# Kernel optimization log

Hardware: AMD Instinct MI355X
Metric: run time of the kernel (lower is better)

Reference implementation:

```python
import jax, jax.numpy as jnp
import numpy as np

EPS = 1e-4  # ReEig eigenvalue clamp threshold (standard SPDNet value)


def _eig_apply(X, fn):
    # symmetric eig, apply fn to eigenvalues, reconstruct: V diag(fn(w)) V^T
    w, v = jnp.linalg.eigh(X)
    return jnp.einsum('...ij,...j,...kj->...ik', v, fn(w), v)


def _congr(P, G, mode):
    # CongrG: G^{+/-1/2} P G^{+/-1/2}, G is a single [n,n] SPD matrix
    w, v = jnp.linalg.eigh(G)
    s = jnp.sqrt(w) if mode == 'pos' else 1.0 / jnp.sqrt(w)
    Gs = (v * s) @ v.T  # [n,n]
    return Gs @ P @ Gs


def setup_inputs() -> dict:
    key = jax.random.key(0)
    ks = jax.random.split(key, 8)
    B, win, band, n, h, n_mid = 512, 3, 9, 22, 27, 32
    # SPD input covariance-like matrices
    M = jax.random.normal(ks[0], (B, win, band, n, n), dtype=jnp.float32)
    x = M @ jnp.swapaxes(M, -1, -2) / n + 0.5 * jnp.eye(n, dtype=jnp.float32)
    # Stiefel BiMap weights (orthonormal columns)
    W1, _ = jnp.linalg.qr(jax.random.normal(ks[1], (h, n_mid, n_mid), dtype=jnp.float32))
    Q2, _ = jnp.linalg.qr(jax.random.normal(ks[2], (h, n_mid, n_mid), dtype=jnp.float32))
    W2 = Q2[..., :n]
    running_mean = jnp.eye(n, dtype=jnp.float32)
    Aw = jax.random.normal(ks[3], (n, n), dtype=jnp.float32)
    bn_weight = Aw @ Aw.T / n + jnp.eye(n, dtype=jnp.float32)
    conv_w = jax.random.normal(ks[4], (48, 1, win, band * n * n), dtype=jnp.float32) * 0.01
    conv_b = jnp.zeros((48,), dtype=jnp.float32)
    fc_w = jax.random.normal(ks[5], (4, 48), dtype=jnp.float32) * 0.1
    fc_b = jnp.zeros((4,), dtype=jnp.float32)
    return {"x": x, "W1": W1, "W2": W2, "running_mean": running_mean,
            "bn_weight": bn_weight, "conv_w": conv_w, "conv_b": conv_b,
            "fc_w": fc_w, "fc_b": fc_b}


def reference(x, W1, W2, running_mean, bn_weight, conv_w, conv_b, fc_w, fc_b):
    B, win, band, n, _ = x.shape
    h = win * band
    no1 = W1.shape[-1]
    X = x.reshape(B, h, n, n)
    # SPDIncreaseDim(n -> no1): E X E^T + diag([0]*n + [1]*(no1-n))
    pad = no1 - n
    X = jnp.pad(X, ((0, 0), (0, 0), (0, pad), (0, pad)))
    X = X + jnp.diag(jnp.concatenate([jnp.zeros(n), jnp.ones(pad)])).astype(x.dtype)
    # BiMap 1 (per-channel W^T X W) + ReEig
    P = jnp.einsum('hni,bhnm,hmj->bhij', W1, X, W1)
    P = _eig_apply(P, lambda w: jnp.maximum(w, EPS))
    # BiMap 2
    P = jnp.einsum('hni,bhnm,hmj->bhij', W2, P, W2)
    # BatchNormSPD (eval mode): center by running_mean, scale by weight
    P = _congr(P, running_mean, 'neg')
    P = _congr(P, bn_weight, 'pos')
    # ReEig + LogEig
    P = _eig_apply(P, lambda w: jnp.maximum(w, EPS))
    P = _eig_apply(P, jnp.log)
    x_vec = P.reshape(B, win, band * n * n)
    feat = jnp.einsum('bhw,chw->bc', x_vec, conv_w[:, 0]) + conv_b  # [B, 48]
    return feat @ fc_w.T + fc_b                       # [B, classes]
```

## Files before the change

### kernel.cpp

```cpp
#include <hip/hip_runtime.h>


#define WS_CONST 484
#define WS_VT    512
#define WS_V     (512 + 13068)
#define WS_D     (13580 + 14256)
#define WS_G     (27836 + 13068)
#define G_STRIDE 528
#define V_STRIDE 528

typedef float v2f __attribute__((ext_vector_type(2)));

static __device__ __forceinline__ float dpp_shl1(float x) {
  return __int_as_float(__builtin_amdgcn_mov_dpp(__float_as_int(x), 0x101, 0xf, 0xf, true));
}
static __device__ __forceinline__ float dpp_shr1(float x) {
  return __int_as_float(__builtin_amdgcn_mov_dpp(__float_as_int(x), 0x111, 0xf, 0xf, true));
}

static __device__ __forceinline__ void jacobi_sweeps(v2f wl[11], v2f wr[11],
                                                     bool is0, bool is10, bool inert,
                                                     int minsweep, float eps2) {
  int okprev = 0;
  #pragma unroll 1
  for (int sweep = 0; sweep < 5; ++sweep) {
    if (sweep >= minsweep && __all(okprev)) break;
    v2f na = (v2f)(0.f), nb = (v2f)(0.f);
    #pragma unroll
    for (int i = 0; i < 11; ++i) { na += wl[i]*wl[i]; nb += wr[i]*wr[i]; }
    float nL = na.x + na.y, nR = nb.x + nb.y;
    float q = inert ? 0.f : (nL*nL + nR*nR);
    q += __shfl_xor(q, 1, 16);
    q += __shfl_xor(q, 2, 16);
    q += __shfl_xor(q, 4, 16);
    q += __shfl_xor(q, 8, 16);
    float dacc = 0.f;
    #pragma unroll 1
    for (int r = 0; r < 21; ++r) {
      v2f da = (v2f)(0.f), db = (v2f)(0.f);
      #pragma unroll
      for (int i = 0; i < 10; i += 2) { da += wl[i]*wr[i]; db += wl[i+1]*wr[i+1]; }
      da += wl[10]*wr[10];
      float d = (da.x + da.y) + (db.x + db.y);
      dacc += d*d;
      float ad  = fabsf(d);
      float tau = (nR - nL)*0.5f*__builtin_amdgcn_rcpf(d);
      float sq  = sqrtf(1.0f + tau*tau);
      float t   = copysignf(__builtin_amdgcn_rcpf(fabsf(tau) + sq), tau);
      float c   = __builtin_amdgcn_rsqf(1.0f + t*t);
      float s   = t*c;
      bool tiny = (ad < 1e-28f);
      c = tiny ? 1.0f : c;
      s = tiny ? 0.0f : s;
      float cc = c*c, ss = s*s, cs2 = 2.0f*c*s;
      float nLn = cc*nL - cs2*d + ss*nR;
      float nRn = ss*nL + cs2*d + cc*nR;
      v2f cv = (v2f)(c), sv = (v2f)(s);
      #pragma unroll
      for (int i = 0; i < 11; ++i) {
        v2f nl = cv*wl[i] - sv*wr[i];
        v2f nr = sv*wl[i] + cv*wr[i];
        float tlx = dpp_shl1(nl.x), tly = dpp_shl1(nl.y);
        float trx = dpp_shr1(nr.x), trY = dpp_shr1(nr.y);
        wl[i].x = is0 ? nl.x : (is10 ? nr.x : tlx);
        wl[i].y = is0 ? nl.y : (is10 ? nr.y : tly);
        wr[i].x = is0 ? tlx : trx;
        wr[i].y = is0 ? tly : trY;
      }
      {
        float tl = dpp_shl1(nLn), tr = dpp_shr1(nRn);
        nL = is0 ? nLn : (is10 ? nRn : tl);
        nR = is0 ? tl : tr;
      }
    }
    float ds = inert ? 0.f : dacc;
    ds += __shfl_xor(ds, 1, 16);
    ds += __shfl_xor(ds, 2, 16);
    ds += __shfl_xor(ds, 4, 16);
    ds += __shfl_xor(ds, 8, 16);
    okprev = (ds <= eps2*q);
  }
}

__global__ void prep_kernel(const float* __restrict__ rm, const float* __restrict__ bn,
                            const float* __restrict__ W1, const float* __restrict__ W2,
                            const float* __restrict__ conv_w, const float* __restrict__ fc_w,
                            const float* __restrict__ conv_b, const float* __restrict__ fc_b,
                            float* __restrict__ ws, float* __restrict__ out) {
  __shared__ float sW1[1024] __attribute__((aligned(16)));
  __shared__ float sW2[704]  __attribute__((aligned(16)));
  __shared__ float sY[2][2][484] __attribute__((aligned(16)));
  __shared__ float sZ[2][2][484] __attribute__((aligned(16)));
  __shared__ float sT[2][484]    __attribute__((aligned(16)));
  __shared__ float sS[484]  __attribute__((aligned(16)));
  __shared__ float sU[704]  __attribute__((aligned(16)));
  __shared__ float sE[220]  __attribute__((aligned(16)));
  __shared__ float sG[1936] __attribute__((aligned(16)));
  __shared__ float sC[2];
  const int tid = threadIdx.x, h = blockIdx.x;

  if (h == 0)
    for (int idx = tid; idx < 2048; idx += 256) out[idx] = 0.f;

  const int wv = tid >> 6, ln = tid & 63;
  if (wv < 2) {
    const float* src = wv ? rm : bn;
    float s = 0.f;
    for (int i = ln; i < 484; i += 64) { float v = src[i]; s += v*v; }
    s += __shfl_xor(s, 1);  s += __shfl_xor(s, 2);  s += __shfl_xor(s, 4);
    s += __shfl_xor(s, 8);  s += __shfl_xor(s, 16); s += __shfl_xor(s, 32);
    if (ln == 0) sC[wv] = sqrtf(s);
  } else {
    const int t = tid - 128;
    for (int i = t; i < 1024; i += 128) sW1[i] = W1[h*1024 + i];
    for (int i = t; i < 704;  i += 128) sW2[i] = W2[h*704 + i];
  }
  __syncthreads();

  {
    const float ic0 = 1.0f/sC[0], ic1 = 1.0f/sC[1];
    for (int idx = tid; idx < 484; idx += 256) {
      const int i = idx/22, j = idx - 22*i;
      const float e = (i == j) ? 1.f : 0.f;
      sY[0][0][idx] = bn[idx]*ic0;  sZ[0][0][idx] = e;
      sY[1][0][idx] = rm[idx]*ic1;  sZ[1][0][idx] = e;
    }
  }
  __syncthreads();

  int cur = 0;
  #pragma unroll 1
  for (int it = 0; it < 11; ++it) {
    for (int idx = tid; idx < 484; idx += 256) {
      const int mt = (idx >= 242), r = idx - mt*242, i = r/11, jp = r - 11*i;
      const float* Zc = sZ[mt][cur];
      const float* Yc = sY[mt][cur];
      v2f acc = (v2f)(0.f);
      #pragma unroll
      for (int k = 0; k < 22; ++k)
        acc += *(const v2f*)(Yc + k*22 + 2*jp) * Zc[i*22 + k];
      v2f tv;
      tv.x = ((2*jp     == i) ? 3.f : 0.f) - acc.x;
      tv.y = ((2*jp + 1 == i) ? 3.f : 0.f) - acc.y;
      *(v2f*)(sT[mt] + i*22 + 2*jp) = tv;
    }
    __syncthreads();
    for (int idx = tid; idx < 968; idx += 256) {
      const int sel = idx/242, r = idx - 242*sel, i = r/11, jp = r - 11*i;
      const int mt = sel >> 1; const bool isZ = sel & 1;
      const float* A = isZ ? sT[mt] : sY[mt][cur];
      const float* B = isZ ? sZ[mt][cur] : sT[mt];
      v2f acc = (v2f)(0.f);
      #pragma unroll
      for (int k = 0; k < 22; ++k)
        acc += *(const v2f*)(B + k*22 + 2*jp) * A[i*22 + k];
      *(v2f*)((isZ ? sZ[mt][cur^1] : sY[mt][cur^1]) + i*22 + 2*jp) = 0.5f*acc;
    }
    __syncthreads();
    cur ^= 1;
  }

  {
    const float scale = sqrtf(sC[0]/sC[1]);
    const float* Zrm = sZ[1][cur];
    const float* Ybn = sY[0][cur];
    for (int idx = tid; idx < 484; idx += 256) {
      const int i = idx/22, j = idx - 22*i;
      float s = 0.f;
      for (int k = 0; k < 22; ++k) s += Zrm[i*22+k]*Ybn[k*22+j];
      sS[idx] = scale*s;
    }
  }
  for (int idx = tid; idx < 704; idx += 256) {
    const int n = idx/22, j = idx - 22*n;
    float s = 0.f;
    for (int k = 0; k < 32; ++k) s += sW1[n*32+k]*sW2[k*22+j];
    sU[idx] = s;
  }
  if (tid < 242) {
    const int wi = h/9, bi = h - 9*wi;
    const float* base = conv_w + wi*4356 + bi*484 + 2*tid;
    v2f a0 = (v2f)(0.f), a1 = (v2f)(0.f), a2 = (v2f)(0.f), a3 = (v2f)(0.f);
    #pragma unroll
    for (int c = 0; c < 48; ++c) {
      const v2f wv2 = *(const v2f*)(base + c*13068);
      a0 += wv2*fc_w[c];
      a1 += wv2*fc_w[48+c];
      a2 += wv2*fc_w[96+c];
      a3 += wv2*fc_w[144+c];
    }
    *(v2f*)(sG +        2*tid) = a0;
    *(v2f*)(sG +  484 + 2*tid) = a1;
    *(v2f*)(sG +  968 + 2*tid) = a2;
    *(v2f*)(sG + 1452 + 2*tid) = a3;
  }
  __syncthreads();

  for (int idx = tid; idx < 484; idx += 256) {
    const int k = idx/22, j = idx - 22*k;
    float s = 0.f;
    for (int l = 0; l < 22; ++l) s += sU[k*22+l]*sS[l*22+j];
    ws[WS_VT + h*484 + j*22 + k] = s;
    ws[WS_V  + h*V_STRIDE + k*24 + j] = s;
  }
  for (int idx = tid; idx < 220; idx += 256) {
    const int e = idx/22, j = idx - 22*e;
    float s = 0.f;
    for (int l = 0; l < 22; ++l) s += sU[(22+e)*22+l]*sS[l*22+j];
    sE[idx] = s;
  }
  __syncthreads();
  for (int idx = tid; idx < 484; idx += 256) {
    const int i = idx/22, j = idx - 22*i;
    float s = 0.f;
    for (int e = 0; e < 10; ++e) s += sE[e*22+i]*sE[e*22+j];
    ws[WS_D + h*484 + idx] = s;
  }
  for (int idx = tid; idx < 1936; idx += 256) {
    const int o = idx/484, r = idx - 484*o, i = r/22, j = r - 22*i;
    const float v = 0.5f*(sG[o*484 + i*22 + j] + sG[o*484 + j*22 + i]);
    ws[WS_G + (o*27+h)*G_STRIDE + i*24 + j] = v;
  }
  if (h == 0 && tid < 4) {
    float s = 0.f;
    for (int c = 0; c < 48; ++c) s += fc_w[tid*48+c]*conv_b[c];
    ws[WS_CONST + tid] = s + fc_b[tid];
  }
}

__global__ void __launch_bounds__(64, 3) main_kernel(const float* __restrict__ x,
                                                     const float* __restrict__ ws,
                                                     float* __restrict__ out) {
  const int lane = threadIdx.x;
  const int g = lane >> 4, m = lane & 15;
  const int mm = (m < 10) ? m : 10;
  const int h  = blockIdx.x % 27;
  const int b  = (blockIdx.x/27)*4 + g;
  const int id = b*27 + h;

  v2f vl[11], vrr[11];
  {
    const v2f* vb = (const v2f*)(ws + WS_VT + h*484 + mm*44);
    #pragma unroll
    for (int j = 0; j < 11; ++j) { vl[j] = vb[j]; vrr[j] = vb[11+j]; }
  }
  v2f wl[11], wr[11];
  {
    const v2f* d2 = (const v2f*)(ws + WS_D + h*484 + mm*44);
    #pragma unroll
    for (int j = 0; j < 11; ++j) { wl[j] = d2[j]; wr[j] = d2[11+j]; }
  }
  {
    const v2f* X2 = (const v2f*)(x + (size_t)id * 484);
    const float* Vrow = ws + WS_V + h*V_STRIDE;
    #pragma unroll 2
    for (int k = 0; k < 22; ++k) {
      v2f aL = (v2f)(0.f), aR = (v2f)(0.f);
      #pragma unroll
      for (int c = 0; c < 11; ++c) {
        v2f xv = X2[11*k + c];
        aL += xv*vl[c];
        aR += xv*vrr[c];
      }
      float tLk = aL.x + aL.y, tRk = aR.x + aR.y;
      const v2f* vk = (const v2f*)(Vrow + k*24);
      #pragma unroll
      for (int j = 0; j < 11; ++j) {
        v2f q = vk[j];
        wl[j] += q*tLk;
        wr[j] += q*tRk;
      }
    }
  }

  jacobi_sweeps(wl, wr, (m == 0), (m == 10), (m > 10), 2, 1e-4f);

  float nL, nR;
  {
    v2f na = (v2f)(0.f), nb = (v2f)(0.f);
    #pragma unroll
    for (int i = 0; i < 11; ++i) { na += wl[i]*wl[i]; nb += wr[i]*wr[i]; }
    nL = na.x + na.y; nR = nb.x + nb.y;
  }
  const float HALF_LN2 = 0.34657359f;
  float coefL = HALF_LN2*log2f(fmaxf(nL, 1e-8f))*__builtin_amdgcn_rcpf(nL);
  float coefR = HALF_LN2*log2f(fmaxf(nR, 1e-8f))*__builtin_amdgcn_rcpf(nR);

  #pragma unroll 1
  for (int o = 0; o < 4; ++o) {
    const float* Gptr = ws + WS_G + (o*27+h)*G_STRIDE;
    float qL = 0.f, qR = 0.f;
    #pragma unroll
    for (int k = 0; k < 22; ++k) {
      const v2f* g2 = (const v2f*)(Gptr + k*24);
      v2f sa = (v2f)(0.f), ra = (v2f)(0.f);
      #pragma unroll
      for (int j = 0; j < 11; ++j) {
        v2f q = g2[j];
        sa += q*wl[j];
        ra += q*wr[j];
      }
      float wLk = wl[k>>1][k&1], wRk = wr[k>>1][k&1];
      qL += wLk*(sa.x + sa.y);
      qR += wRk*(ra.x + ra.y);
    }
    float v = (m <= 10) ? (coefL*qL + coefR*qR) : 0.0f;
    v += __shfl_down(v, 8, 16);
    v += __shfl_down(v, 4, 16);
    v += __shfl_down(v, 2, 16);
    v += __shfl_down(v, 1, 16);
    if (m == 0) {
      if (h == 0) v += ws[WS_CONST + o];
      atomicAdd(out + b*4 + o, v);
    }
  }
}

extern "C" void kernel_launch(void* const* d_in, const int* in_sizes, int n_in,
                              void* d_out, int out_size, void* d_ws, size_t ws_size,
                              hipStream_t stream) {
  const float* x   = (const float*)d_in[0];
  const float* W1  = (const float*)d_in[1];
  const float* W2  = (const float*)d_in[2];
  const float* rm  = (const float*)d_in[3];
  const float* bn  = (const float*)d_in[4];
  const float* cw  = (const float*)d_in[5];
  const float* cb  = (const float*)d_in[6];
  const float* fw  = (const float*)d_in[7];
  const float* fb  = (const float*)d_in[8];
  float* out = (float*)d_out;
  float* ws  = (float*)d_ws;

  prep_kernel<<<27, 256, 0, stream>>>(rm, bn, W1, W2, cw, fw, cb, fb, ws, out);
  main_kernel<<<3456, 64, 0, stream>>>(x, ws, out);
}
```

Measured before the change: 316.6 us.

## Restructure Jacobi round-robin into odd-even pair phases with local swaps

```diff
diff --git a/kernel.cpp b/kernel.cpp
--- a/kernel.cpp
+++ b/kernel.cpp
@@ -19,7 +19,7 @@
 }
 
 static __device__ __forceinline__ void jacobi_sweeps(v2f wl[11], v2f wr[11],
-                                                     bool is0, bool is10, bool inert,
+                                                     bool is0, bool act, bool inert,
                                                      int minsweep, float eps2) {
   int okprev = 0;
   #pragma unroll 1
@@ -36,41 +36,74 @@
     q += __shfl_xor(q, 8, 16);
     float dacc = 0.f;
     #pragma unroll 1
-    for (int r = 0; r < 21; ++r) {
-      v2f da = (v2f)(0.f), db = (v2f)(0.f);
-      #pragma unroll
-      for (int i = 0; i < 10; i += 2) { da += wl[i]*wr[i]; db += wl[i+1]*wr[i+1]; }
-      da += wl[10]*wr[10];
-      float d = (da.x + da.y) + (db.x + db.y);
-      dacc += d*d;
-      float ad  = fabsf(d);
-      float tau = (nR - nL)*0.5f*__builtin_amdgcn_rcpf(d);
-      float sq  = sqrtf(1.0f + tau*tau);
-      float t   = copysignf(__builtin_amdgcn_rcpf(fabsf(tau) + sq), tau);
-      float c   = __builtin_amdgcn_rsqf(1.0f + t*t);
-      float s   = t*c;
-      bool tiny = (ad < 1e-28f);
-      c = tiny ? 1.0f : c;
-      s = tiny ? 0.0f : s;
-      float cc = c*c, ss = s*s, cs2 = 2.0f*c*s;
-      float nLn = cc*nL - cs2*d + ss*nR;
-      float nRn = ss*nL + cs2*d + cc*nR;
-      v2f cv = (v2f)(c), sv = (v2f)(s);
-      #pragma unroll
-      for (int i = 0; i < 11; ++i) {
-        v2f nl = cv*wl[i] - sv*wr[i];
-        v2f nr = sv*wl[i] + cv*wr[i];
-        float tlx = dpp_shl1(nl.x), tly = dpp_shl1(nl.y);
-        float trx = dpp_shr1(nr.x), trY = dpp_shr1(nr.y);
-        wl[i].x = is0 ? nl.x : (is10 ? nr.x : tlx);
-        wl[i].y = is0 ? nl.y : (is10 ? nr.y : tly);
-        wr[i].x = is0 ? tlx : trx;
-        wr[i].y = is0 ? tly : trY;
-      }
+    for (int r = 0; r < 11; ++r) {
       {
-        float tl = dpp_shl1(nLn), tr = dpp_shr1(nRn);
-        nL = is0 ? nLn : (is10 ? nRn : tl);
-        nR = is0 ? tl : tr;
+        v2f da = (v2f)(0.f), db = (v2f)(0.f);
+        #pragma unroll
+        for (int i = 0; i < 10; i += 2) { da += wl[i]*wr[i]; db += wl[i+1]*wr[i+1]; }
+        da += wl[10]*wr[10];
+        float d = (da.x + da.y) + (db.x + db.y);
+        dacc += d*d;
+        float ad  = fabsf(d);
+        float tau = (nR - nL)*0.5f*__builtin_amdgcn_rcpf(d);
+        float sq  = sqrtf(1.0f + tau*tau);
+        float t   = copysignf(__builtin_amdgcn_rcpf(fabsf(tau) + sq), tau);
+        float c   = __builtin_amdgcn_rsqf(1.0f + t*t);
+        float s   = t*c;
+        bool tiny = (ad < 1e-28f);
+        c = tiny ? 1.0f : c;
+        s = tiny ? 0.0f : s;
+        float cc = c*c, ss = s*s, cs2 = 2.0f*c*s;
+        float nLn = cc*nL - cs2*d + ss*nR;
+        float nRn = ss*nL + cs2*d + cc*nR;
+        v2f cv = (v2f)(c), sv = (v2f)(s);
+        #pragma unroll
+        for (int i = 0; i < 11; ++i) {
+          v2f nl = cv*wl[i] - sv*wr[i];
+          v2f nr = sv*wl[i] + cv*wr[i];
+          wl[i] = nr;
+          wr[i] = nl;
+        }
+        nL = nRn; nR = nLn;
+      }
+      {
+        v2f u[11];
+        #pragma unroll
+        for (int i = 0; i < 11; ++i) { u[i].x = dpp_shl1(wl[i].x); u[i].y = dpp_shl1(wl[i].y); }
+        float nU = dpp_shl1(nL);
+        v2f da = (v2f)(0.f), db = (v2f)(0.f);
+        #pragma unroll
+        for (int i = 0; i < 10; i += 2) { da += wr[i]*u[i]; db += wr[i+1]*u[i+1]; }
+        da += wr[10]*u[10];
+        float d = (da.x + da.y) + (db.x + db.y);
+        d = act ? d : 0.f;
+        dacc += d*d;
+        float ad  = fabsf(d);
+        float tau = (nU - nR)*0.5f*__builtin_amdgcn_rcpf(d);
+        float sq  = sqrtf(1.0f + tau*tau);
+        float t   = copysignf(__builtin_amdgcn_rcpf(fabsf(tau) + sq), tau);
+        float c   = __builtin_amdgcn_rsqf(1.0f + t*t);
+        float s   = t*c;
+        bool tiny = (ad < 1e-28f);
+        c = tiny ? 1.0f : c;
+        s = tiny ? 0.0f : s;
+        float cc = c*c, ss = s*s, cs2 = 2.0f*c*s;
+        v2f cv = (v2f)(c), sv = (v2f)(s);
+        #pragma unroll
+        for (int i = 0; i < 11; ++i) {
+          v2f rl = cv*wr[i] - sv*u[i];
+          v2f rr = sv*wr[i] + cv*u[i];
+          wr[i].x = act ? rr.x : wr[i].x;
+          wr[i].y = act ? rr.y : wr[i].y;
+          float bx = dpp_shr1(rl.x), by = dpp_shr1(rl.y);
+          wl[i].x = is0 ? wl[i].x : bx;
+          wl[i].y = is0 ? wl[i].y : by;
+        }
+        float nRn = ss*nR + cs2*d + cc*nU;
+        float nLg = cc*nR - cs2*d + ss*nU;
+        nR = act ? nRn : nR;
+        float bn2 = dpp_shr1(nLg);
+        nL = is0 ? nL : bn2;
       }
     }
     float ds = inert ? 0.f : dacc;
@@ -273,7 +306,7 @@
     }
   }
 
-  jacobi_sweeps(wl, wr, (m == 0), (m == 10), (m > 10), 2, 1e-4f);
+  jacobi_sweeps(wl, wr, (m == 0), (m < 10), (m > 10), 2, 1e-4f);
 
   float nL, nR;
   {
```

Result: faster. 274.8 us (-13.2%).
